# Kernel tuning notes

Hardware: AMD Instinct MI355X
Metric: run time of the kernel (lower is better)

## Reference

```python
import jax, jax.numpy as jnp
import numpy as np

DIM, HEADS, DIM_HEAD = 1024, 16, 64
DIM_INNER = HEADS * DIM_HEAD  # 1024
SCALE = DIM_HEAD ** -0.5


def _rope(t):
    # t: [b, h, n, d]; interleaved-pair RoPE (lucidrains rotary-embedding-torch default)
    d = t.shape[-1]
    n = t.shape[-2]
    inv_freq = 1.0 / (10000.0 ** (jnp.arange(0, d, 2, dtype=jnp.float32) / d))
    angles = jnp.arange(n, dtype=jnp.float32)[:, None] * inv_freq[None, :]  # [n, d/2]
    cos, sin = jnp.cos(angles), jnp.sin(angles)
    t1, t2 = t[..., 0::2], t[..., 1::2]
    r1 = t1 * cos - t2 * sin
    r2 = t1 * sin + t2 * cos
    return jnp.stack([r1, r2], axis=-1).reshape(t.shape)


def setup_inputs() -> dict:
    key = jax.random.key(0)
    ks = jax.random.split(key, 8)
    b, n = 2, 2048
    inp = {
        "x": jax.random.normal(ks[0], (b, n, DIM), dtype=jnp.float32),
        "value_residual": jax.random.normal(ks[1], (b, HEADS, n, DIM_HEAD), dtype=jnp.float32),
        "gamma": jnp.ones((DIM,), dtype=jnp.float32),
        "w_qkv": jax.random.normal(ks[2], (DIM, 3 * DIM_INNER), dtype=jnp.float32) * (DIM ** -0.5),
        "w_mix": jax.random.normal(ks[3], (DIM, HEADS), dtype=jnp.float32) * (DIM ** -0.5),
        "b_mix": jnp.zeros((HEADS,), dtype=jnp.float32),
        "w_gates": jax.random.normal(ks[4], (DIM, HEADS), dtype=jnp.float32) * (DIM ** -0.5),
        "b_gates": jnp.zeros((HEADS,), dtype=jnp.float32),
        "w_out": jax.random.normal(ks[5], (DIM_INNER, DIM), dtype=jnp.float32) * (DIM_INNER ** -0.5),
    }
    return inp


def reference(x, value_residual, gamma, w_qkv, w_mix, b_mix, w_gates, b_gates, w_out):
    b, n, _ = x.shape
    # RMSNorm (lucidrains style: F.normalize * sqrt(dim) * gamma)
    norm = jnp.sqrt(jnp.sum(x * x, axis=-1, keepdims=True))
    xn = x / jnp.maximum(norm, 1e-12) * (DIM ** 0.5) * gamma

    qkv = xn @ w_qkv  # [b, n, 3*h*d]
    qkv = qkv.reshape(b, n, 3, HEADS, DIM_HEAD)
    q, k, v = [jnp.transpose(qkv[:, :, i], (0, 2, 1, 3)) for i in range(3)]  # [b,h,n,d]
    original_values = v

    # learned value-residual lerp
    mix = jax.nn.sigmoid(xn @ w_mix + b_mix)            # [b, n, h]
    mix = jnp.transpose(mix, (0, 2, 1))[..., None]       # [b, h, n, 1]
    v = v * (1.0 - mix) + value_residual * mix

    # rotary on q, k
    q = _rope(q)
    k = _rope(k)

    scores = jnp.einsum("bhid,bhjd->bhij", q, k) * SCALE
    attn = jax.nn.softmax(scores, axis=-1)
    out = jnp.einsum("bhij,bhjd->bhid", attn, v)         # [b, h, n, d]

    gates = jax.nn.sigmoid(xn @ w_gates + b_gates)       # [b, n, h]
    out = out * jnp.transpose(gates, (0, 2, 1))[..., None]

    out = jnp.transpose(out, (0, 2, 1, 3)).reshape(b, n, DIM_INNER)
    return out @ w_out, original_values
```

## Files before the change

kernel.cpp:

```cpp
#include <hip/hip_runtime.h>
#include <hip/hip_bf16.h>
#include <math.h>

#define DIMSZ 1024
#define HEADS 16
#define DHEAD 64
#define NSEQ  2048
#define BATCH 2
#define ROWS  (BATCH*NSEQ)
#define SCALE 0.125f
#define LOG2E 1.4426950408889634f

typedef __attribute__((ext_vector_type(8))) short short8;
typedef __attribute__((ext_vector_type(4))) float floatx4;

#define MFMA16(a,b,c) __builtin_amdgcn_mfma_f32_16x16x32_bf16(a,b,c,0,0,0)

__device__ __forceinline__ void gl2lds16(const void* g, void* l) {
    __builtin_amdgcn_global_load_lds(
        (const __attribute__((address_space(1))) unsigned int*)g,
        (__attribute__((address_space(3))) unsigned int*)l, 16, 0, 0);
}

__device__ __forceinline__ unsigned short bf16r(float a) {
    unsigned u = __float_as_uint(a);
    u += 0x7fff + ((u >> 16) & 1);
    return (unsigned short)(u >> 16);
}
__device__ __forceinline__ unsigned pack_bf16(float a, float b) {
    unsigned ua = __float_as_uint(a), ub = __float_as_uint(b);
    ua += 0x7fff + ((ua >> 16) & 1);
    ub += 0x7fff + ((ub >> 16) & 1);
    return (ua >> 16) | (ub & 0xffff0000u);
}
__device__ __forceinline__ float2 bf2f(unsigned u) {
    float2 r;
    r.x = __uint_as_float(u << 16);
    r.y = __uint_as_float(u & 0xffff0000u);
    return r;
}
__device__ __forceinline__ float fexp2(float x) {
#if __has_builtin(__builtin_amdgcn_exp2f)
    return __builtin_amdgcn_exp2f(x);
#else
    return exp2f(x);
#endif
}
__device__ __forceinline__ unsigned short f2bf(float f) {
    __hip_bfloat16 h = __float2bfloat16(f);
    return *(unsigned short*)&h;
}

__global__ __launch_bounds__(256) void transpose_bf16_kernel(
    const float* __restrict__ src, unsigned short* __restrict__ dst, int K, int N)
{
    __shared__ float t[32][33];
    const int tx = threadIdx.x & 31, tyy = threadIdx.x >> 5;
    const int n0 = blockIdx.x * 32, k0 = blockIdx.y * 32;
    #pragma unroll
    for (int i = 0; i < 4; i++)
        t[tyy*4 + i][tx] = src[(size_t)(k0 + tyy*4 + i)*N + n0 + tx];
    __syncthreads();
    #pragma unroll
    for (int i = 0; i < 4; i++)
        dst[(size_t)(n0 + tyy*4 + i)*K + k0 + tx] = f2bf(t[tx][tyy*4 + i]);
}

__global__ __launch_bounds__(256) void rmsnorm_mix_kernel(
    const float* __restrict__ x, const float* __restrict__ gamma,
    const float* __restrict__ w_mix, const float* __restrict__ b_mix,
    const float* __restrict__ w_gates, const float* __restrict__ b_gates,
    unsigned short* __restrict__ xnb, float* __restrict__ mixo, float* __restrict__ gateso)
{
    const int row = blockIdx.x;
    const int tid = threadIdx.x;
    __shared__ float xs[DIMSZ];
    __shared__ float red[16][17];
    __shared__ float wred[4];

    const float4 xv = ((const float4*)(x + (size_t)row * DIMSZ))[tid];
    float ss = xv.x*xv.x + xv.y*xv.y + xv.z*xv.z + xv.w*xv.w;
    #pragma unroll
    for (int off = 1; off < 64; off <<= 1) ss += __shfl_xor(ss, off);
    if ((tid & 63) == 0) wred[tid >> 6] = ss;
    __syncthreads();
    const float total = wred[0] + wred[1] + wred[2] + wred[3];
    const float inv = 32.0f / fmaxf(sqrtf(total), 1e-12f);
    const float4 gv = ((const float4*)gamma)[tid];
    float4 o;
    o.x = xv.x * inv * gv.x; o.y = xv.y * inv * gv.y;
    o.z = xv.z * inv * gv.z; o.w = xv.w * inv * gv.w;
    uint2 pk;
    pk.x = pack_bf16(o.x, o.y);
    pk.y = pack_bf16(o.z, o.w);
    ((uint2*)(xnb + (size_t)row * DIMSZ))[tid] = pk;
    ((float4*)xs)[tid] = o;
    __syncthreads();

    const int h = tid & 15, chunk = tid >> 4;
    float pm = 0.f, pg = 0.f;
    #pragma unroll 8
    for (int j = 0; j < 64; j++) {
        const int d = chunk * 64 + j;
        const float xv_ = xs[d];
        pm += xv_ * w_mix[d * HEADS + h];
        pg += xv_ * w_gates[d * HEADS + h];
    }
    red[chunk][h] = pm;
    __syncthreads();
    if (tid < HEADS) {
        float s = 0.f;
        #pragma unroll
        for (int c = 0; c < 16; c++) s += red[c][tid];
        mixo[(size_t)row * HEADS + tid] = 1.0f / (1.0f + __expf(-(s + b_mix[tid])));
    }
    __syncthreads();
    red[chunk][h] = pg;
    __syncthreads();
    if (tid < HEADS) {
        float s = 0.f;
        #pragma unroll
        for (int c = 0; c < 16; c++) s += red[c][tid];
        gateso[(size_t)row * HEADS + tid] = 1.0f / (1.0f + __expf(-(s + b_gates[tid])));
    }
}

__global__ __launch_bounds__(256) void gemm_qkv_mfma(
    const unsigned short* __restrict__ A, const unsigned short* __restrict__ BT,
    unsigned short* __restrict__ qb, unsigned short* __restrict__ kb,
    float* __restrict__ vb)
{
    __shared__ short As[128*32];
    __shared__ short Bs[128*32];
    const int tid = threadIdx.x;
    const int wv = tid >> 6, lane = tid & 63;
    const int g = lane >> 4, c = lane & 15;
    const int wm = wv >> 1, wn = wv & 1;
    const int bm = blockIdx.y * 128, bn = blockIdx.x * 128;

    floatx4 acc[4][4];
    #pragma unroll
    for (int mt = 0; mt < 4; mt++)
        #pragma unroll
        for (int nt = 0; nt < 4; nt++) acc[mt][nt] = (floatx4){0.f,0.f,0.f,0.f};

    for (int k0 = 0; k0 < DIMSZ; k0 += 32) {
        __syncthreads();
        #pragma unroll
        for (int r = 0; r < 2; r++) {
            const int ch = tid + 256*r;
            const int row = ch >> 2, cc = ch & 3;
            gl2lds16(A  + (size_t)(bm + row)*DIMSZ + k0 + cc*8, (void*)(As + ch*8));
            gl2lds16(BT + (size_t)(bn + row)*DIMSZ + k0 + cc*8, (void*)(Bs + ch*8));
        }
        __syncthreads();
        short8 af[4], bf[4];
        #pragma unroll
        for (int mt = 0; mt < 4; mt++) af[mt] = *(const short8*)(As + (wm*64 + mt*16 + c)*32 + g*8);
        #pragma unroll
        for (int nt = 0; nt < 4; nt++) bf[nt] = *(const short8*)(Bs + (wn*64 + nt*16 + c)*32 + g*8);
        #pragma unroll
        for (int mt = 0; mt < 4; mt++)
            #pragma unroll
            for (int nt = 0; nt < 4; nt++)
                acc[mt][nt] = MFMA16(af[mt], bf[nt], acc[mt][nt]);
    }
    const int i3 = bn >> 10;
    const int nb = bn - (i3 << 10);
    if (i3 < 2) {
        unsigned short* dst = (i3 == 0) ? qb : kb;
        #pragma unroll
        for (int mt = 0; mt < 4; mt++)
            #pragma unroll
            for (int nt = 0; nt < 4; nt++)
                #pragma unroll
                for (int r2 = 0; r2 < 4; r2++) {
                    const int row = bm + wm*64 + mt*16 + g*4 + r2;
                    const int col = nb + wn*64 + nt*16 + c;
                    const int hh = col >> 6, dd = col & 63;
                    const int bb2 = row >> 11, pos = row & 2047;
                    dst[(((size_t)(bb2*HEADS + hh)*NSEQ) + pos)*DHEAD + dd] = bf16r(acc[mt][nt][r2]);
                }
    } else {
        #pragma unroll
        for (int mt = 0; mt < 4; mt++)
            #pragma unroll
            for (int nt = 0; nt < 4; nt++)
                #pragma unroll
                for (int r2 = 0; r2 < 4; r2++) {
                    const int row = bm + wm*64 + mt*16 + g*4 + r2;
                    const int col = nb + wn*64 + nt*16 + c;
                    const int hh = col >> 6, dd = col & 63;
                    const int bb2 = row >> 11, pos = row & 2047;
                    vb[(((size_t)(bb2*HEADS + hh)*NSEQ) + pos)*DHEAD + dd] = acc[mt][nt][r2];
                }
    }
}

__global__ __launch_bounds__(256) void rope_blend_kernel2(
    unsigned short* __restrict__ q, unsigned short* __restrict__ k,
    const float* __restrict__ vorig, const float* __restrict__ vres,
    const float* __restrict__ mixb, unsigned short* __restrict__ vT)
{
    __shared__ unsigned short vt[64*72];
    const int tid = threadIdx.x;
    const int bh = blockIdx.y, bb = bh >> 4, h = bh & 15;
    const int p0 = blockIdx.x * 64;
    {
        const int pr = tid >> 2, d0 = (tid & 3) * 16;
        const int pos = p0 + pr;
        const size_t base = ((size_t)bh*NSEQ + pos)*DHEAD + d0;

        uint4 qr0 = *(uint4*)(q + base), qr1 = *(uint4*)(q + base + 8);
        uint4 kr0 = *(uint4*)(k + base), kr1 = *(uint4*)(k + base + 8);
        unsigned qw[8] = {qr0.x, qr0.y, qr0.z, qr0.w, qr1.x, qr1.y, qr1.z, qr1.w};
        unsigned kw[8] = {kr0.x, kr0.y, kr0.z, kr0.w, kr1.x, kr1.y, kr1.z, kr1.w};
        const float QSC = SCALE * LOG2E;
        #pragma unroll
        for (int j = 0; j < 8; j++) {
            const int p = (d0 >> 1) + j;
            const float invf = powf(10000.0f, -(float)(2*p) * (1.0f/64.0f));
            float sn, cs;
            sincosf((float)pos * invf, &sn, &cs);
            float2 qv = bf2f(qw[j]);
            float2 kv = bf2f(kw[j]);
            const float q1 = qv.x*cs - qv.y*sn, q2 = qv.x*sn + qv.y*cs;
            const float k1 = kv.x*cs - kv.y*sn, k2 = kv.x*sn + kv.y*cs;
            qw[j] = pack_bf16(q1*QSC, q2*QSC);
            kw[j] = pack_bf16(k1, k2);
        }
        *(uint4*)(q + base)     = *(uint4*)(qw + 0);
        *(uint4*)(q + base + 8) = *(uint4*)(qw + 4);
        *(uint4*)(k + base)     = *(uint4*)(kw + 0);
        *(uint4*)(k + base + 8) = *(uint4*)(kw + 4);

        float vv[16], vr[16];
        #pragma unroll
        for (int i = 0; i < 4; i++) {
            *(float4*)(vv + i*4) = *(const float4*)(vorig + base + i*4);
            *(float4*)(vr + i*4) = *(const float4*)(vres + base + i*4);
        }
        const float mx = mixb[((size_t)(bb*NSEQ + pos))*HEADS + h];
        #pragma unroll
        for (int j = 0; j < 8; j++) {
            const float b0 = vv[2*j]*(1.f-mx)   + vr[2*j]*mx;
            const float b1 = vv[2*j+1]*(1.f-mx) + vr[2*j+1]*mx;
            vt[pr*72 + d0 + 2*j]     = bf16r(b0);
            vt[pr*72 + d0 + 2*j + 1] = bf16r(b1);
        }
    }
    __syncthreads();
    {
        const int dd = tid >> 2, c0 = (tid & 3) * 16;
        unsigned o[8];
        #pragma unroll
        for (int j = 0; j < 8; j++) {
            const unsigned a  = vt[(c0 + 2*j)*72 + dd];
            const unsigned b2 = vt[(c0 + 2*j + 1)*72 + dd];
            o[j] = a | (b2 << 16);
        }
        unsigned short* dst = vT + ((size_t)bh*DHEAD + dd)*NSEQ + p0 + c0;
        *(uint4*)(dst)     = *(uint4*)(o + 0);
        *(uint4*)(dst + 8) = *(uint4*)(o + 4);
    }
}

__global__ __launch_bounds__(256) void attn_mfma_kernel(
    const unsigned short* __restrict__ qg,
    const unsigned short* __restrict__ kg,
    const unsigned short* __restrict__ vT,
    const float* __restrict__ gates,
    unsigned short* __restrict__ outp)
{
    __shared__ short Kt[64*64];
    __shared__ short Vt[64*64];
    __shared__ short Ps[4*32*64];

    const int tid = threadIdx.x;
    const int w = tid >> 6, lane = tid & 63;
    const int g = lane >> 4, c = lane & 15;
    const int bh = blockIdx.y, bb = bh >> 4, h = bh & 15;
    const int q0 = blockIdx.x * 128;

    short8 qf[2][2];
    #pragma unroll
    for (int mt = 0; mt < 2; mt++)
        #pragma unroll
        for (int kb = 0; kb < 2; kb++)
            qf[mt][kb] = *(const short8*)(qg + ((size_t)bh*NSEQ + q0 + w*32 + mt*16 + c)*DHEAD + kb*32 + g*8);

    floatx4 O[2][4];
    #pragma unroll
    for (int mt = 0; mt < 2; mt++)
        #pragma unroll
        for (int nt = 0; nt < 4; nt++) O[mt][nt] = (floatx4){0.f,0.f,0.f,0.f};
    float lsum[2] = {0.f, 0.f};

    short* PsW = Ps + w * (32*64);
    const unsigned short* kbase = kg + (size_t)bh*NSEQ*DHEAD;
    const unsigned short* vbase = vT + (size_t)bh*DHEAD*NSEQ;

    for (int kt = 0; kt < NSEQ/64; kt++) {
        __syncthreads();
        #pragma unroll
        for (int r = 0; r < 2; r++) {
            const int ch = tid + 256*r;
            const int row = ch >> 3;
            const int u = (ch & 7) ^ (row & 7);
            gl2lds16(kbase + (size_t)(kt*64 + row)*DHEAD + u*8, (void*)(Kt + ch*8));
            gl2lds16(vbase + (size_t)row*NSEQ + kt*64 + u*8,   (void*)(Vt + ch*8));
        }
        __syncthreads();

        short8 kfr[4][2];
        #pragma unroll
        for (int nt = 0; nt < 4; nt++) {
            const int rowk = nt*16 + c;
            #pragma unroll
            for (int kb = 0; kb < 2; kb++)
                kfr[nt][kb] = *(const short8*)(Kt + rowk*64 + (((kb*4 + g) ^ (rowk & 7)) * 8));
        }

        #pragma unroll
        for (int mt = 0; mt < 2; mt++) {
            const int rr = mt*16 + c;
            #pragma unroll
            for (int nt = 0; nt < 4; nt++) {
                floatx4 accS = (floatx4){0.f,0.f,0.f,0.f};
                #pragma unroll
                for (int kb = 0; kb < 2; kb++)
                    accS = MFMA16(kfr[nt][kb], qf[mt][kb], accS);
                const float p0 = fexp2(accS[0]);
                const float p1 = fexp2(accS[1]);
                const float p2 = fexp2(accS[2]);
                const float p3 = fexp2(accS[3]);
                lsum[mt] += (p0 + p1) + (p2 + p3);
                uint2 pk;
                pk.x = pack_bf16(p0, p1);
                pk.y = pack_bf16(p2, p3);
                *(uint2*)(PsW + rr*64 + (((nt*2 + (g >> 1)) ^ (rr & 7)) * 8) + (g & 1)*4) = pk;
            }
        }
        __builtin_amdgcn_s_waitcnt(0xc07f);
        #pragma unroll
        for (int kb = 0; kb < 2; kb++) {
            short8 pf[2];
            #pragma unroll
            for (int mt = 0; mt < 2; mt++) {
                const int rr = mt*16 + c;
                pf[mt] = *(const short8*)(PsW + rr*64 + (((kb*4 + g) ^ (rr & 7)) * 8));
            }
            #pragma unroll
            for (int nt = 0; nt < 4; nt++) {
                const int rv = nt*16 + c;
                short8 vf = *(const short8*)(Vt + rv*64 + (((kb*4 + g) ^ (rv & 7)) * 8));
                #pragma unroll
                for (int mt = 0; mt < 2; mt++)
                    O[mt][nt] = MFMA16(pf[mt], vf, O[mt][nt]);
            }
        }
    }

    #pragma unroll
    for (int mt = 0; mt < 2; mt++) {
        float l = lsum[mt];
        l += __shfl_xor(l, 16);
        l += __shfl_xor(l, 32);
        #pragma unroll
        for (int r2 = 0; r2 < 4; r2++) {
            const float lr = __shfl(l, g*4 + r2);
            const int rowg = q0 + w*32 + mt*16 + g*4 + r2;
            const float gt = gates[((size_t)(bb*NSEQ + rowg))*HEADS + h];
            const float sc = gt / lr;
            unsigned short* op = outp + ((size_t)(bb*NSEQ + rowg))*DIMSZ + h*DHEAD + c;
            #pragma unroll
            for (int nt = 0; nt < 4; nt++)
                op[nt*16] = bf16r(O[mt][nt][r2] * sc);
        }
    }
}

__global__ __launch_bounds__(256) void gemm_out_mfma(
    const unsigned short* __restrict__ A, const unsigned short* __restrict__ BT,
    float* __restrict__ out0)
{
    __shared__ short As[128*32];
    __shared__ short Bs[128*32];
    const int tid = threadIdx.x;
    const int wv = tid >> 6, lane = tid & 63;
    const int g = lane >> 4, c = lane & 15;
    const int wm = wv >> 1, wn = wv & 1;
    const int bm = blockIdx.y * 128, bn = blockIdx.x * 128;

    floatx4 acc[4][4];
    #pragma unroll
    for (int mt = 0; mt < 4; mt++)
        #pragma unroll
        for (int nt = 0; nt < 4; nt++) acc[mt][nt] = (floatx4){0.f,0.f,0.f,0.f};

    for (int k0 = 0; k0 < DIMSZ; k0 += 32) {
        __syncthreads();
        #pragma unroll
        for (int r = 0; r < 2; r++) {
            const int ch = tid + 256*r;
            const int row = ch >> 2, cc = ch & 3;
            gl2lds16(A  + (size_t)(bm + row)*DIMSZ + k0 + cc*8, (void*)(As + ch*8));
            gl2lds16(BT + (size_t)(bn + row)*DIMSZ + k0 + cc*8, (void*)(Bs + ch*8));
        }
        __syncthreads();
        short8 af[4], bf[4];
        #pragma unroll
        for (int mt = 0; mt < 4; mt++) af[mt] = *(const short8*)(As + (wm*64 + mt*16 + c)*32 + g*8);
        #pragma unroll
        for (int nt = 0; nt < 4; nt++) bf[nt] = *(const short8*)(Bs + (wn*64 + nt*16 + c)*32 + g*8);
        #pragma unroll
        for (int mt = 0; mt < 4; mt++)
            #pragma unroll
            for (int nt = 0; nt < 4; nt++)
                acc[mt][nt] = MFMA16(af[mt], bf[nt], acc[mt][nt]);
    }
    #pragma unroll
    for (int mt = 0; mt < 4; mt++)
        #pragma unroll
        for (int nt = 0; nt < 4; nt++)
            #pragma unroll
            for (int r2 = 0; r2 < 4; r2++) {
                const int row = bm + wm*64 + mt*16 + g*4 + r2;
                const int col = bn + wn*64 + nt*16 + c;
                out0[(size_t)row*DIMSZ + col] = acc[mt][nt][r2];
            }
}

extern "C" void kernel_launch(void* const* d_in, const int* in_sizes, int n_in,
                              void* d_out, int out_size, void* d_ws, size_t ws_size,
                              hipStream_t stream) {
    const float* x       = (const float*)d_in[0];
    const float* vres    = (const float*)d_in[1];
    const float* gamma   = (const float*)d_in[2];
    const float* w_qkv   = (const float*)d_in[3];
    const float* w_mix   = (const float*)d_in[4];
    const float* b_mix   = (const float*)d_in[5];
    const float* w_gates = (const float*)d_in[6];
    const float* b_gates = (const float*)d_in[7];
    const float* w_out   = (const float*)d_in[8];

    float* out0 = (float*)d_out;
    float* out1 = out0 + (size_t)ROWS * DIMSZ;

    char* ws = (char*)d_ws;
    unsigned short* xnb   = (unsigned short*)(ws);
    unsigned short* wqkvT = (unsigned short*)(ws + (8u<<20));
    unsigned short* woutT = (unsigned short*)(ws + (14u<<20));
    unsigned short* qb2   = (unsigned short*)(ws + (16u<<20));
    unsigned short* kb2   = (unsigned short*)(ws + (24u<<20));
    unsigned short* vT    = (unsigned short*)(ws + (32u<<20));
    unsigned short* attnO = (unsigned short*)(ws + (40u<<20));
    float*          mixb  = (float*)(ws + (48u<<20));
    float*          gatesb= (float*)(ws + (48u<<20) + 262144);

    transpose_bf16_kernel<<<dim3(3*DIMSZ/32, DIMSZ/32), 256, 0, stream>>>(
        w_qkv, wqkvT, DIMSZ, 3*DIMSZ);
    transpose_bf16_kernel<<<dim3(DIMSZ/32, DIMSZ/32), 256, 0, stream>>>(
        w_out, woutT, DIMSZ, DIMSZ);

    rmsnorm_mix_kernel<<<ROWS, 256, 0, stream>>>(
        x, gamma, w_mix, b_mix, w_gates, b_gates, xnb, mixb, gatesb);

    gemm_qkv_mfma<<<dim3(3*DIMSZ/128, ROWS/128), 256, 0, stream>>>(
        xnb, wqkvT, qb2, kb2, out1);

    rope_blend_kernel2<<<dim3(NSEQ/64, BATCH*HEADS), 256, 0, stream>>>(
        qb2, kb2, out1, vres, mixb, vT);

    attn_mfma_kernel<<<dim3(NSEQ/128, BATCH*HEADS), 256, 0, stream>>>(
        qb2, kb2, vT, gatesb, attnO);

    gemm_out_mfma<<<dim3(DIMSZ/128, ROWS/128), 256, 0, stream>>>(
        attnO, woutT, out0);
}
```

Measured before the change: 272.1 us.

## Halve attention query tile, merge weight transposes, use fast hardware sin/cos in RoPE

The attention kernel now handles 64 queries per block (16 per wave) instead of 128, which doubles the grid to 1024 blocks for better CU occupancy, at the cost of loading each K/V tile twice as often. The two weight-transpose launches are merged into one kernel, and rounding is switched to the inline bf16r helper. RoPE replaces powf/sincosf with exp2 plus the hardware sin/cos on fractional revolutions, which is cheaper but less precise.

```diff
diff --git a/kernel.cpp b/kernel.cpp
--- a/kernel.cpp
+++ b/kernel.cpp
@@ -46,24 +46,41 @@
     return exp2f(x);
 #endif
 }
-__device__ __forceinline__ unsigned short f2bf(float f) {
-    __hip_bfloat16 h = __float2bfloat16(f);
-    return *(unsigned short*)&h;
-}
-
-__global__ __launch_bounds__(256) void transpose_bf16_kernel(
-    const float* __restrict__ src, unsigned short* __restrict__ dst, int K, int N)
+__device__ __forceinline__ float fsin_rev(float x) {
+#if __has_builtin(__builtin_amdgcn_sinf)
+    return __builtin_amdgcn_sinf(x);
+#else
+    return __sinf(x * 6.28318530717958647692f);
+#endif
+}
+__device__ __forceinline__ float fcos_rev(float x) {
+#if __has_builtin(__builtin_amdgcn_cosf)
+    return __builtin_amdgcn_cosf(x);
+#else
+    return __cosf(x * 6.28318530717958647692f);
+#endif
+}
+
+__global__ __launch_bounds__(256) void transpose_both_kernel(
+    const float* __restrict__ w_qkv, const float* __restrict__ w_out,
+    unsigned short* __restrict__ wqkvT, unsigned short* __restrict__ woutT)
 {
     __shared__ float t[32][33];
     const int tx = threadIdx.x & 31, tyy = threadIdx.x >> 5;
-    const int n0 = blockIdx.x * 32, k0 = blockIdx.y * 32;
+    const int bx = blockIdx.x;
+    const float* src;
+    unsigned short* dst;
+    int N, n0;
+    if (bx < 96) { src = w_qkv; dst = wqkvT; N = 3*DIMSZ; n0 = bx*32; }
+    else         { src = w_out; dst = woutT; N = DIMSZ;   n0 = (bx-96)*32; }
+    const int k0 = blockIdx.y * 32;
     #pragma unroll
     for (int i = 0; i < 4; i++)
         t[tyy*4 + i][tx] = src[(size_t)(k0 + tyy*4 + i)*N + n0 + tx];
     __syncthreads();
     #pragma unroll
     for (int i = 0; i < 4; i++)
-        dst[(size_t)(n0 + tyy*4 + i)*K + k0 + tx] = f2bf(t[tx][tyy*4 + i]);
+        dst[(size_t)(n0 + tyy*4 + i)*DIMSZ + k0 + tx] = bf16r(t[tx][tyy*4 + i]);
 }
 
 __global__ __launch_bounds__(256) void rmsnorm_mix_kernel(
@@ -216,12 +233,15 @@
         unsigned qw[8] = {qr0.x, qr0.y, qr0.z, qr0.w, qr1.x, qr1.y, qr1.z, qr1.w};
         unsigned kw[8] = {kr0.x, kr0.y, kr0.z, kr0.w, kr1.x, kr1.y, kr1.z, kr1.w};
         const float QSC = SCALE * LOG2E;
+        const float posf = (float)pos;
         #pragma unroll
         for (int j = 0; j < 8; j++) {
-            const int p = (d0 >> 1) + j;
-            const float invf = powf(10000.0f, -(float)(2*p) * (1.0f/64.0f));
-            float sn, cs;
-            sincosf((float)pos * invf, &sn, &cs);
+            const float pf = (float)((d0 >> 1) + j);
+            const float rev = posf * fexp2(-pf * 0.41524101186092029f
+                                           - 2.6514961294723187f);
+            const float rf = rev - floorf(rev);
+            const float sn = fsin_rev(rf);
+            const float cs = fcos_rev(rf);
             float2 qv = bf2f(qw[j]);
             float2 kv = bf2f(kw[j]);
             const float q1 = qv.x*cs - qv.y*sn, q2 = qv.x*sn + qv.y*cs;
@@ -274,31 +294,28 @@
 {
     __shared__ short Kt[64*64];
     __shared__ short Vt[64*64];
-    __shared__ short Ps[4*32*64];
+    __shared__ short Ps[4*16*64];
 
     const int tid = threadIdx.x;
     const int w = tid >> 6, lane = tid & 63;
     const int g = lane >> 4, c = lane & 15;
     const int bh = blockIdx.y, bb = bh >> 4, h = bh & 15;
-    const int q0 = blockIdx.x * 128;
-
-    short8 qf[2][2];
-    #pragma unroll
-    for (int mt = 0; mt < 2; mt++)
-        #pragma unroll
-        for (int kb = 0; kb < 2; kb++)
-            qf[mt][kb] = *(const short8*)(qg + ((size_t)bh*NSEQ + q0 + w*32 + mt*16 + c)*DHEAD + kb*32 + g*8);
-
-    floatx4 O[2][4];
-    #pragma unroll
-    for (int mt = 0; mt < 2; mt++)
-        #pragma unroll
-        for (int nt = 0; nt < 4; nt++) O[mt][nt] = (floatx4){0.f,0.f,0.f,0.f};
-    float lsum[2] = {0.f, 0.f};
-
-    short* PsW = Ps + w * (32*64);
+    const int q0 = blockIdx.x * 64;
+
+    short8 qf[2];
+    #pragma unroll
+    for (int kb = 0; kb < 2; kb++)
+        qf[kb] = *(const short8*)(qg + ((size_t)bh*NSEQ + q0 + w*16 + c)*DHEAD + kb*32 + g*8);
+
+    floatx4 O[4];
+    #pragma unroll
+    for (int nt = 0; nt < 4; nt++) O[nt] = (floatx4){0.f,0.f,0.f,0.f};
+    float lsum = 0.f;
+
+    short* PsW = Ps + w * (16*64);
     const unsigned short* kbase = kg + (size_t)bh*NSEQ*DHEAD;
     const unsigned short* vbase = vT + (size_t)bh*DHEAD*NSEQ;
+    const int rr = c;
 
     for (int kt = 0; kt < NSEQ/64; kt++) {
         __syncthreads();
@@ -312,71 +329,51 @@
         }
         __syncthreads();
 
-        short8 kfr[4][2];
         #pragma unroll
         for (int nt = 0; nt < 4; nt++) {
             const int rowk = nt*16 + c;
-            #pragma unroll
-            for (int kb = 0; kb < 2; kb++)
-                kfr[nt][kb] = *(const short8*)(Kt + rowk*64 + (((kb*4 + g) ^ (rowk & 7)) * 8));
-        }
-
-        #pragma unroll
-        for (int mt = 0; mt < 2; mt++) {
-            const int rr = mt*16 + c;
-            #pragma unroll
-            for (int nt = 0; nt < 4; nt++) {
-                floatx4 accS = (floatx4){0.f,0.f,0.f,0.f};
-                #pragma unroll
-                for (int kb = 0; kb < 2; kb++)
-                    accS = MFMA16(kfr[nt][kb], qf[mt][kb], accS);
-                const float p0 = fexp2(accS[0]);
-                const float p1 = fexp2(accS[1]);
-                const float p2 = fexp2(accS[2]);
-                const float p3 = fexp2(accS[3]);
-                lsum[mt] += (p0 + p1) + (p2 + p3);
-                uint2 pk;
-                pk.x = pack_bf16(p0, p1);
-                pk.y = pack_bf16(p2, p3);
-                *(uint2*)(PsW + rr*64 + (((nt*2 + (g >> 1)) ^ (rr & 7)) * 8) + (g & 1)*4) = pk;
+            floatx4 accS = (floatx4){0.f,0.f,0.f,0.f};
+            #pragma unroll
+            for (int kb = 0; kb < 2; kb++) {
+                short8 kfr = *(const short8*)(Kt + rowk*64 + (((kb*4 + g) ^ (rowk & 7)) * 8));
+                accS = MFMA16(kfr, qf[kb], accS);
             }
+            const float p0 = fexp2(accS[0]);
+            const float p1 = fexp2(accS[1]);
+            const float p2 = fexp2(accS[2]);
+            const float p3 = fexp2(accS[3]);
+            lsum += (p0 + p1) + (p2 + p3);
+            uint2 pk;
+            pk.x = pack_bf16(p0, p1);
+            pk.y = pack_bf16(p2, p3);
+            *(uint2*)(PsW + rr*64 + (((nt*2 + (g >> 1)) ^ (rr & 7)) * 8) + (g & 1)*4) = pk;
         }
         __builtin_amdgcn_s_waitcnt(0xc07f);
         #pragma unroll
         for (int kb = 0; kb < 2; kb++) {
-            short8 pf[2];
-            #pragma unroll
-            for (int mt = 0; mt < 2; mt++) {
-                const int rr = mt*16 + c;
-                pf[mt] = *(const short8*)(PsW + rr*64 + (((kb*4 + g) ^ (rr & 7)) * 8));
-            }
+            short8 pf = *(const short8*)(PsW + rr*64 + (((kb*4 + g) ^ (rr & 7)) * 8));
             #pragma unroll
             for (int nt = 0; nt < 4; nt++) {
                 const int rv = nt*16 + c;
                 short8 vf = *(const short8*)(Vt + rv*64 + (((kb*4 + g) ^ (rv & 7)) * 8));
-                #pragma unroll
-                for (int mt = 0; mt < 2; mt++)
-                    O[mt][nt] = MFMA16(pf[mt], vf, O[mt][nt]);
+                O[nt] = MFMA16(pf, vf, O[nt]);
             }
         }
     }
 
-    #pragma unroll
-    for (int mt = 0; mt < 2; mt++) {
-        float l = lsum[mt];
-        l += __shfl_xor(l, 16);
-        l += __shfl_xor(l, 32);
-        #pragma unroll
-        for (int r2 = 0; r2 < 4; r2++) {
-            const float lr = __shfl(l, g*4 + r2);
-            const int rowg = q0 + w*32 + mt*16 + g*4 + r2;
-            const float gt = gates[((size_t)(bb*NSEQ + rowg))*HEADS + h];
-            const float sc = gt / lr;
-            unsigned short* op = outp + ((size_t)(bb*NSEQ + rowg))*DIMSZ + h*DHEAD + c;
-            #pragma unroll
-            for (int nt = 0; nt < 4; nt++)
-                op[nt*16] = bf16r(O[mt][nt][r2] * sc);
-        }
+    float l = lsum;
+    l += __shfl_xor(l, 16);
+    l += __shfl_xor(l, 32);
+    #pragma unroll
+    for (int r2 = 0; r2 < 4; r2++) {
+        const float lr = __shfl(l, g*4 + r2);
+        const int rowg = q0 + w*16 + g*4 + r2;
+        const float gt = gates[((size_t)(bb*NSEQ + rowg))*HEADS + h];
+        const float sc = gt / lr;
+        unsigned short* op = outp + ((size_t)(bb*NSEQ + rowg))*DIMSZ + h*DHEAD + c;
+        #pragma unroll
+        for (int nt = 0; nt < 4; nt++)
+            op[nt*16] = bf16r(O[nt][r2] * sc);
     }
 }
 
@@ -458,10 +455,8 @@
     float*          mixb  = (float*)(ws + (48u<<20));
     float*          gatesb= (float*)(ws + (48u<<20) + 262144);
 
-    transpose_bf16_kernel<<<dim3(3*DIMSZ/32, DIMSZ/32), 256, 0, stream>>>(
-        w_qkv, wqkvT, DIMSZ, 3*DIMSZ);
-    transpose_bf16_kernel<<<dim3(DIMSZ/32, DIMSZ/32), 256, 0, stream>>>(
-        w_out, woutT, DIMSZ, DIMSZ);
+    transpose_both_kernel<<<dim3(128, DIMSZ/32), 256, 0, stream>>>(
+        w_qkv, w_out, wqkvT, woutT);
 
     rmsnorm_mix_kernel<<<ROWS, 256, 0, stream>>>(
         x, gamma, w_mix, b_mix, w_gates, b_gates, xnb, mixb, gatesb);
@@ -472,7 +467,7 @@
     rope_blend_kernel2<<<dim3(NSEQ/64, BATCH*HEADS), 256, 0, stream>>>(
         qb2, kb2, out1, vres, mixb, vT);
 
-    attn_mfma_kernel<<<dim3(NSEQ/128, BATCH*HEADS), 256, 0, stream>>>(
+    attn_mfma_kernel<<<dim3(NSEQ/64, BATCH*HEADS), 256, 0, stream>>>(
         qb2, kb2, vT, gatesb, attnO);
 
     gemm_out_mfma<<<dim3(DIMSZ/128, ROWS/128), 256, 0, stream>>>(
```

After: 269.1 us. No clear change (-1.1%).

## Split attention KV across wave groups, MFMA mix/gates, merge transposes, fast RoPE

Applied to the files above, without the earlier changes.

Attention blocks now run 512 threads. Two wave groups each process half of the key sequence and their partial outputs and row sums are combined through LDS at the end. This doubles the parallelism per query tile, which matters because the grid has only 512 blocks. The mix/gate projections move from a scalar per-row loop into a separate bf16 MFMA GEMM. The three weight transposes are merged into one launch. The q/k GEMM epilogue is staged through LDS so it can issue 16-byte stores. RoPE replaces powf/sincosf with exp2 and hardware sin/cos in revolutions, which reduces precision and lowers mix/gate precision to bf16.

```diff
diff --git a/kernel.cpp b/kernel.cpp
--- a/kernel.cpp
+++ b/kernel.cpp
@@ -46,36 +46,64 @@
     return exp2f(x);
 #endif
 }
-__device__ __forceinline__ unsigned short f2bf(float f) {
-    __hip_bfloat16 h = __float2bfloat16(f);
-    return *(unsigned short*)&h;
-}
-
-__global__ __launch_bounds__(256) void transpose_bf16_kernel(
-    const float* __restrict__ src, unsigned short* __restrict__ dst, int K, int N)
+__device__ __forceinline__ float fsin_rev(float x) {
+#if __has_builtin(__builtin_amdgcn_sinf)
+    return __builtin_amdgcn_sinf(x);
+#else
+    return __sinf(x * 6.28318530717958647692f);
+#endif
+}
+__device__ __forceinline__ float fcos_rev(float x) {
+#if __has_builtin(__builtin_amdgcn_cosf)
+    return __builtin_amdgcn_cosf(x);
+#else
+    return __cosf(x * 6.28318530717958647692f);
+#endif
+}
+
+__global__ __launch_bounds__(256) void transpose_all_kernel(
+    const float* __restrict__ w_qkv, const float* __restrict__ w_out,
+    const float* __restrict__ w_mix, const float* __restrict__ w_gates,
+    unsigned short* __restrict__ wqkvT, unsigned short* __restrict__ woutT,
+    unsigned short* __restrict__ wmgT)
 {
     __shared__ float t[32][33];
     const int tx = threadIdx.x & 31, tyy = threadIdx.x >> 5;
-    const int n0 = blockIdx.x * 32, k0 = blockIdx.y * 32;
-    #pragma unroll
-    for (int i = 0; i < 4; i++)
-        t[tyy*4 + i][tx] = src[(size_t)(k0 + tyy*4 + i)*N + n0 + tx];
-    __syncthreads();
-    #pragma unroll
-    for (int i = 0; i < 4; i++)
-        dst[(size_t)(n0 + tyy*4 + i)*K + k0 + tx] = f2bf(t[tx][tyy*4 + i]);
-}
-
-__global__ __launch_bounds__(256) void rmsnorm_mix_kernel(
+    const int bx = blockIdx.x;
+    const int k0 = blockIdx.y * 32;
+    if (bx < 128) {
+        const float* src;
+        unsigned short* dst;
+        int N, n0;
+        if (bx < 96) { src = w_qkv; dst = wqkvT; N = 3*DIMSZ; n0 = bx*32; }
+        else         { src = w_out; dst = woutT; N = DIMSZ;   n0 = (bx-96)*32; }
+        #pragma unroll
+        for (int i = 0; i < 4; i++)
+            t[tyy*4 + i][tx] = src[(size_t)(k0 + tyy*4 + i)*N + n0 + tx];
+        __syncthreads();
+        #pragma unroll
+        for (int i = 0; i < 4; i++)
+            dst[(size_t)(n0 + tyy*4 + i)*DIMSZ + k0 + tx] = bf16r(t[tx][tyy*4 + i]);
+    } else {
+        #pragma unroll
+        for (int i = 0; i < 4; i++) {
+            const int kk = k0 + tyy*4 + i;
+            t[tyy*4 + i][tx] = (tx < 16) ? w_mix[kk*16 + tx]
+                                         : w_gates[kk*16 + (tx - 16)];
+        }
+        __syncthreads();
+        #pragma unroll
+        for (int i = 0; i < 4; i++)
+            wmgT[(size_t)(tyy*4 + i)*DIMSZ + k0 + tx] = bf16r(t[tx][tyy*4 + i]);
+    }
+}
+
+__global__ __launch_bounds__(256) void rmsnorm_kernel(
     const float* __restrict__ x, const float* __restrict__ gamma,
-    const float* __restrict__ w_mix, const float* __restrict__ b_mix,
-    const float* __restrict__ w_gates, const float* __restrict__ b_gates,
-    unsigned short* __restrict__ xnb, float* __restrict__ mixo, float* __restrict__ gateso)
+    unsigned short* __restrict__ xnb)
 {
     const int row = blockIdx.x;
     const int tid = threadIdx.x;
-    __shared__ float xs[DIMSZ];
-    __shared__ float red[16][17];
     __shared__ float wred[4];
 
     const float4 xv = ((const float4*)(x + (size_t)row * DIMSZ))[tid];
@@ -87,42 +115,63 @@
     const float total = wred[0] + wred[1] + wred[2] + wred[3];
     const float inv = 32.0f / fmaxf(sqrtf(total), 1e-12f);
     const float4 gv = ((const float4*)gamma)[tid];
-    float4 o;
-    o.x = xv.x * inv * gv.x; o.y = xv.y * inv * gv.y;
-    o.z = xv.z * inv * gv.z; o.w = xv.w * inv * gv.w;
     uint2 pk;
-    pk.x = pack_bf16(o.x, o.y);
-    pk.y = pack_bf16(o.z, o.w);
+    pk.x = pack_bf16(xv.x * inv * gv.x, xv.y * inv * gv.y);
+    pk.y = pack_bf16(xv.z * inv * gv.z, xv.w * inv * gv.w);
     ((uint2*)(xnb + (size_t)row * DIMSZ))[tid] = pk;
-    ((float4*)xs)[tid] = o;
-    __syncthreads();
-
-    const int h = tid & 15, chunk = tid >> 4;
-    float pm = 0.f, pg = 0.f;
-    #pragma unroll 8
-    for (int j = 0; j < 64; j++) {
-        const int d = chunk * 64 + j;
-        const float xv_ = xs[d];
-        pm += xv_ * w_mix[d * HEADS + h];
-        pg += xv_ * w_gates[d * HEADS + h];
-    }
-    red[chunk][h] = pm;
-    __syncthreads();
-    if (tid < HEADS) {
-        float s = 0.f;
-        #pragma unroll
-        for (int c = 0; c < 16; c++) s += red[c][tid];
-        mixo[(size_t)row * HEADS + tid] = 1.0f / (1.0f + __expf(-(s + b_mix[tid])));
-    }
-    __syncthreads();
-    red[chunk][h] = pg;
-    __syncthreads();
-    if (tid < HEADS) {
-        float s = 0.f;
-        #pragma unroll
-        for (int c = 0; c < 16; c++) s += red[c][tid];
-        gateso[(size_t)row * HEADS + tid] = 1.0f / (1.0f + __expf(-(s + b_gates[tid])));
-    }
+}
+
+__global__ __launch_bounds__(256) void mix_gates_mfma(
+    const unsigned short* __restrict__ A, const unsigned short* __restrict__ WG,
+    const float* __restrict__ b_mix, const float* __restrict__ b_gates,
+    float* __restrict__ mixo, float* __restrict__ gateso)
+{
+    __shared__ short As[128*32];
+    __shared__ short Bs[32*32];
+    const int tid = threadIdx.x;
+    const int wv = tid >> 6, lane = tid & 63;
+    const int g = lane >> 4, c = lane & 15;
+    const int bm = blockIdx.x * 128;
+
+    floatx4 acc[2][2];
+    #pragma unroll
+    for (int mt = 0; mt < 2; mt++)
+        #pragma unroll
+        for (int nt = 0; nt < 2; nt++) acc[mt][nt] = (floatx4){0.f,0.f,0.f,0.f};
+
+    for (int k0 = 0; k0 < DIMSZ; k0 += 32) {
+        __syncthreads();
+        #pragma unroll
+        for (int r = 0; r < 2; r++) {
+            const int ch = tid + 256*r;
+            const int row = ch >> 2, cc = ch & 3;
+            gl2lds16(A + (size_t)(bm + row)*DIMSZ + k0 + cc*8, (void*)(As + ch*8));
+        }
+        if (tid < 128)
+            gl2lds16(WG + (size_t)(tid >> 2)*DIMSZ + k0 + (tid & 3)*8, (void*)(Bs + tid*8));
+        __syncthreads();
+        short8 af[2], bf[2];
+        #pragma unroll
+        for (int mt = 0; mt < 2; mt++) af[mt] = *(const short8*)(As + (wv*32 + mt*16 + c)*32 + g*8);
+        #pragma unroll
+        for (int nt = 0; nt < 2; nt++) bf[nt] = *(const short8*)(Bs + (nt*16 + c)*32 + g*8);
+        #pragma unroll
+        for (int mt = 0; mt < 2; mt++)
+            #pragma unroll
+            for (int nt = 0; nt < 2; nt++)
+                acc[mt][nt] = MFMA16(af[mt], bf[nt], acc[mt][nt]);
+    }
+    const float bm_c = b_mix[c], bg_c = b_gates[c];
+    #pragma unroll
+    for (int mt = 0; mt < 2; mt++)
+        #pragma unroll
+        for (int r2 = 0; r2 < 4; r2++) {
+            const int row = bm + wv*32 + mt*16 + g*4 + r2;
+            const float lm = acc[mt][0][r2] + bm_c;
+            const float lg = acc[mt][1][r2] + bg_c;
+            mixo[(size_t)row*HEADS + c]   = 1.0f / (1.0f + fexp2(-lm * LOG2E));
+            gateso[(size_t)row*HEADS + c] = 1.0f / (1.0f + fexp2(-lg * LOG2E));
+        }
 }
 
 __global__ __launch_bounds__(256) void gemm_qkv_mfma(
@@ -165,22 +214,32 @@
             for (int nt = 0; nt < 4; nt++)
                 acc[mt][nt] = MFMA16(af[mt], bf[nt], acc[mt][nt]);
     }
+    __syncthreads();
     const int i3 = bn >> 10;
     const int nb = bn - (i3 << 10);
     if (i3 < 2) {
         unsigned short* dst = (i3 == 0) ? qb : kb;
-        #pragma unroll
-        for (int mt = 0; mt < 4; mt++)
+        short* wbuf = As + wv*1152;
+        const int rd_row = lane >> 2, seg = lane & 3;
+        #pragma unroll
+        for (int mt = 0; mt < 4; mt++) {
             #pragma unroll
             for (int nt = 0; nt < 4; nt++)
                 #pragma unroll
-                for (int r2 = 0; r2 < 4; r2++) {
-                    const int row = bm + wm*64 + mt*16 + g*4 + r2;
-                    const int col = nb + wn*64 + nt*16 + c;
-                    const int hh = col >> 6, dd = col & 63;
-                    const int bb2 = row >> 11, pos = row & 2047;
-                    dst[(((size_t)(bb2*HEADS + hh)*NSEQ) + pos)*DHEAD + dd] = bf16r(acc[mt][nt][r2]);
-                }
+                for (int r2 = 0; r2 < 4; r2++)
+                    wbuf[(g*4 + r2)*72 + nt*16 + c] = (short)bf16r(acc[mt][nt][r2]);
+            __builtin_amdgcn_s_waitcnt(0xc07f);
+            const uint4 v0 = *(const uint4*)&wbuf[rd_row*72 + seg*16];
+            const uint4 v1 = *(const uint4*)&wbuf[rd_row*72 + seg*16 + 8];
+            const int row = bm + wm*64 + mt*16 + rd_row;
+            const int col = nb + wn*64 + seg*16;
+            const int hh = col >> 6, dd = col & 63;
+            const int bb2 = row >> 11, pos = row & 2047;
+            unsigned short* dp = dst + (((size_t)(bb2*HEADS + hh)*NSEQ) + pos)*DHEAD + dd;
+            *(uint4*)dp = v0;
+            *(uint4*)(dp + 8) = v1;
+            __builtin_amdgcn_s_waitcnt(0xc07f);
+        }
     } else {
         #pragma unroll
         for (int mt = 0; mt < 4; mt++)
@@ -216,12 +275,15 @@
         unsigned qw[8] = {qr0.x, qr0.y, qr0.z, qr0.w, qr1.x, qr1.y, qr1.z, qr1.w};
         unsigned kw[8] = {kr0.x, kr0.y, kr0.z, kr0.w, kr1.x, kr1.y, kr1.z, kr1.w};
         const float QSC = SCALE * LOG2E;
+        const float posf = (float)pos;
         #pragma unroll
         for (int j = 0; j < 8; j++) {
-            const int p = (d0 >> 1) + j;
-            const float invf = powf(10000.0f, -(float)(2*p) * (1.0f/64.0f));
-            float sn, cs;
-            sincosf((float)pos * invf, &sn, &cs);
+            const float pf = (float)((d0 >> 1) + j);
+            const float rev = posf * fexp2(-pf * 0.41524101186092029f
+                                           - 2.6514961294723187f);
+            const float rf = rev - floorf(rev);
+            const float sn = fsin_rev(rf);
+            const float cs = fcos_rev(rf);
             float2 qv = bf2f(qw[j]);
             float2 kv = bf2f(kw[j]);
             const float q1 = qv.x*cs - qv.y*sn, q2 = qv.x*sn + qv.y*cs;
@@ -265,19 +327,22 @@
     }
 }
 
-__global__ __launch_bounds__(256) void attn_mfma_kernel(
+__global__ __launch_bounds__(512) void attn_mfma_kernel(
     const unsigned short* __restrict__ qg,
     const unsigned short* __restrict__ kg,
     const unsigned short* __restrict__ vT,
     const float* __restrict__ gates,
     unsigned short* __restrict__ outp)
 {
-    __shared__ short Kt[64*64];
-    __shared__ short Vt[64*64];
-    __shared__ short Ps[4*32*64];
+    __shared__ short KV[16384];
+    __shared__ short Ps[16384];
+
+    short* Kt = KV;
+    short* Vt = KV + 8192;
 
     const int tid = threadIdx.x;
     const int w = tid >> 6, lane = tid & 63;
+    const int wq = w & 3, s = w >> 2;
     const int g = lane >> 4, c = lane & 15;
     const int bh = blockIdx.y, bb = bh >> 4, h = bh & 15;
     const int q0 = blockIdx.x * 128;
@@ -287,7 +352,7 @@
     for (int mt = 0; mt < 2; mt++)
         #pragma unroll
         for (int kb = 0; kb < 2; kb++)
-            qf[mt][kb] = *(const short8*)(qg + ((size_t)bh*NSEQ + q0 + w*32 + mt*16 + c)*DHEAD + kb*32 + g*8);
+            qf[mt][kb] = *(const short8*)(qg + ((size_t)bh*NSEQ + q0 + wq*32 + mt*16 + c)*DHEAD + kb*32 + g*8);
 
     floatx4 O[2][4];
     #pragma unroll
@@ -296,19 +361,24 @@
         for (int nt = 0; nt < 4; nt++) O[mt][nt] = (floatx4){0.f,0.f,0.f,0.f};
     float lsum[2] = {0.f, 0.f};
 
-    short* PsW = Ps + w * (32*64);
+    short* PsW = Ps + w * 2048;
+    short* Kts = Kt + s * 4096;
+    short* Vts = Vt + s * 4096;
     const unsigned short* kbase = kg + (size_t)bh*NSEQ*DHEAD;
     const unsigned short* vbase = vT + (size_t)bh*DHEAD*NSEQ;
 
-    for (int kt = 0; kt < NSEQ/64; kt++) {
+    for (int kt2 = 0; kt2 < 16; kt2++) {
         __syncthreads();
         #pragma unroll
         for (int r = 0; r < 2; r++) {
-            const int ch = tid + 256*r;
-            const int row = ch >> 3;
-            const int u = (ch & 7) ^ (row & 7);
-            gl2lds16(kbase + (size_t)(kt*64 + row)*DHEAD + u*8, (void*)(Kt + ch*8));
-            gl2lds16(vbase + (size_t)row*NSEQ + kt*64 + u*8,   (void*)(Vt + ch*8));
+            const int ch = tid + 512*r;
+            const int t  = ch >> 9;
+            const int cw = ch & 511;
+            const int row = cw >> 3;
+            const int u = (cw & 7) ^ (row & 7);
+            const int ktile = kt2 + 16*t;
+            gl2lds16(kbase + (size_t)(ktile*64 + row)*DHEAD + u*8, (void*)(Kt + t*4096 + cw*8));
+            gl2lds16(vbase + (size_t)row*NSEQ + ktile*64 + u*8,   (void*)(Vt + t*4096 + cw*8));
         }
         __syncthreads();
 
@@ -318,7 +388,7 @@
             const int rowk = nt*16 + c;
             #pragma unroll
             for (int kb = 0; kb < 2; kb++)
-                kfr[nt][kb] = *(const short8*)(Kt + rowk*64 + (((kb*4 + g) ^ (rowk & 7)) * 8));
+                kfr[nt][kb] = *(const short8*)(Kts + rowk*64 + (((kb*4 + g) ^ (rowk & 7)) * 8));
         }
 
         #pragma unroll
@@ -353,7 +423,7 @@
             #pragma unroll
             for (int nt = 0; nt < 4; nt++) {
                 const int rv = nt*16 + c;
-                short8 vf = *(const short8*)(Vt + rv*64 + (((kb*4 + g) ^ (rv & 7)) * 8));
+                short8 vf = *(const short8*)(Vts + rv*64 + (((kb*4 + g) ^ (rv & 7)) * 8));
                 #pragma unroll
                 for (int mt = 0; mt < 2; mt++)
                     O[mt][nt] = MFMA16(pf[mt], vf, O[mt][nt]);
@@ -361,21 +431,47 @@
         }
     }
 
-    #pragma unroll
-    for (int mt = 0; mt < 2; mt++) {
-        float l = lsum[mt];
-        l += __shfl_xor(l, 16);
-        l += __shfl_xor(l, 32);
-        #pragma unroll
-        for (int r2 = 0; r2 < 4; r2++) {
-            const float lr = __shfl(l, g*4 + r2);
-            const int rowg = q0 + w*32 + mt*16 + g*4 + r2;
-            const float gt = gates[((size_t)(bb*NSEQ + rowg))*HEADS + h];
-            const float sc = gt / lr;
-            unsigned short* op = outp + ((size_t)(bb*NSEQ + rowg))*DIMSZ + h*DHEAD + c;
+    __syncthreads();
+    float* cb = (float*)KV;
+    float* lf = (float*)Ps;
+    if (s == 1) {
+        #pragma unroll
+        for (int mt = 0; mt < 2; mt++) {
             #pragma unroll
             for (int nt = 0; nt < 4; nt++)
-                op[nt*16] = bf16r(O[mt][nt][r2] * sc);
+                #pragma unroll
+                for (int r2 = 0; r2 < 4; r2++)
+                    cb[wq*2048 + ((mt*4 + nt)*4 + r2)*64 + lane] = O[mt][nt][r2];
+            lf[wq*128 + mt*64 + lane] = lsum[mt];
+        }
+    }
+    __syncthreads();
+    if (s == 0) {
+        #pragma unroll
+        for (int mt = 0; mt < 2; mt++) {
+            #pragma unroll
+            for (int nt = 0; nt < 4; nt++)
+                #pragma unroll
+                for (int r2 = 0; r2 < 4; r2++)
+                    O[mt][nt][r2] += cb[wq*2048 + ((mt*4 + nt)*4 + r2)*64 + lane];
+            lsum[mt] += lf[wq*128 + mt*64 + lane];
+        }
+        #pragma unroll
+        for (int mt = 0; mt < 2; mt++) {
+            float l = lsum[mt];
+            l += __shfl_xor(l, 16);
+            l += __shfl_xor(l, 32);
+            #pragma unroll
+            for (int r2 = 0; r2 < 4; r2++) {
+                const float lr = __shfl(l, g*4 + r2);
+                const int rowg = q0 + wq*32 + mt*16 + g*4 + r2;
+                const float gt = gates[((size_t)(bb*NSEQ + rowg))*HEADS + h];
+                const float sc = gt / lr;
+                unsigned short* op = outp + ((size_t)(bb*NSEQ + rowg))*DIMSZ + h*DHEAD + c;
+                #pragma unroll
+                for (int nt = 0; nt < 4; nt++)
+                    op[nt*16] = bf16r(O[mt][nt][r2] * sc);
+            }
         }
     }
 }
@@ -457,14 +553,15 @@
     unsigned short* attnO = (unsigned short*)(ws + (40u<<20));
     float*          mixb  = (float*)(ws + (48u<<20));
     float*          gatesb= (float*)(ws + (48u<<20) + 262144);
-
-    transpose_bf16_kernel<<<dim3(3*DIMSZ/32, DIMSZ/32), 256, 0, stream>>>(
-        w_qkv, wqkvT, DIMSZ, 3*DIMSZ);
-    transpose_bf16_kernel<<<dim3(DIMSZ/32, DIMSZ/32), 256, 0, stream>>>(
-        w_out, woutT, DIMSZ, DIMSZ);
-
-    rmsnorm_mix_kernel<<<ROWS, 256, 0, stream>>>(
-        x, gamma, w_mix, b_mix, w_gates, b_gates, xnb, mixb, gatesb);
+    unsigned short* wmgT  = (unsigned short*)(ws + (49u<<20));
+
+    transpose_all_kernel<<<dim3(129, DIMSZ/32), 256, 0, stream>>>(
+        w_qkv, w_out, w_mix, w_gates, wqkvT, woutT, wmgT);
+
+    rmsnorm_kernel<<<ROWS, 256, 0, stream>>>(x, gamma, xnb);
+
+    mix_gates_mfma<<<ROWS/128, 256, 0, stream>>>(
+        xnb, wmgT, b_mix, b_gates, mixb, gatesb);
 
     gemm_qkv_mfma<<<dim3(3*DIMSZ/128, ROWS/128), 256, 0, stream>>>(
         xnb, wqkvT, qb2, kb2, out1);
@@ -472,7 +569,7 @@
     rope_blend_kernel2<<<dim3(NSEQ/64, BATCH*HEADS), 256, 0, stream>>>(
         qb2, kb2, out1, vres, mixb, vT);
 
-    attn_mfma_kernel<<<dim3(NSEQ/128, BATCH*HEADS), 256, 0, stream>>>(
+    attn_mfma_kernel<<<dim3(NSEQ/128, BATCH*HEADS), 512, 0, stream>>>(
         qb2, kb2, vT, gatesb, attnO);
 
     gemm_out_mfma<<<dim3(DIMSZ/128, ROWS/128), 256, 0, stream>>>(
```

Result: no change. 276.2 us (+1.5%).
